# Kernel optimization log

Hardware: AMD Instinct MI355X
Metric: run time of the kernel (lower is better)

## Reference

```python
import jax, jax.numpy as jnp
import numpy as np

EPS = 1e-5
DIM = 1024
HEADS = 8
DIM_HEAD = 64
INNER = HEADS * DIM_HEAD  # 512


def layernorm(x, g, b):
    mu = jnp.mean(x, axis=-1, keepdims=True)
    var = jnp.var(x, axis=-1, keepdims=True)
    return (x - mu) * jax.lax.rsqrt(var + EPS) * g + b


def setup_inputs() -> dict:
    key = jax.random.key(0)
    ks = jax.random.split(key, 5)
    b, t, n, m = 4, 4, 2048, 64
    x = jax.random.normal(ks[0], (b, t, n, DIM), dtype=jnp.float32)
    latents = jax.random.normal(ks[1], (b, t, m, DIM), dtype=jnp.float32)
    Wq = jax.random.normal(ks[2], (DIM, INNER), dtype=jnp.float32) * (DIM ** -0.5)
    Wkv = jax.random.normal(ks[3], (DIM, 2 * INNER), dtype=jnp.float32) * (DIM ** -0.5)
    Wo = jax.random.normal(ks[4], (INNER, DIM), dtype=jnp.float32) * (INNER ** -0.5)
    return {
        "x": x, "latents": latents,
        "g_x": jnp.ones((DIM,), jnp.float32), "b_x": jnp.zeros((DIM,), jnp.float32),
        "g_l": jnp.ones((DIM,), jnp.float32), "b_l": jnp.zeros((DIM,), jnp.float32),
        "Wq": Wq, "Wkv": Wkv, "Wo": Wo,
    }


def reference(x, latents, g_x, b_x, g_l, b_l, Wq, Wkv, Wo):
    b, t, n, d = x.shape
    m = latents.shape[2]
    h, dh = HEADS, DIM_HEAD
    scale = dh ** -0.5

    xn = layernorm(x, g_x, b_x)              # (b,t,n,d)
    ln = layernorm(latents, g_l, b_l)        # (b,t,m,d)

    q = jnp.einsum('btmd,de->btme', ln, Wq)  # (b,t,m,inner)
    kv_in = jnp.concatenate([xn, ln], axis=-2)           # (b,t,n+m,d)
    kv = jnp.einsum('btjd,de->btje', kv_in, Wkv)         # (b,t,n+m,2*inner)
    k, v = jnp.split(kv, 2, axis=-1)

    q = q.reshape(b, t, m, h, dh) * scale
    k = k.reshape(b, t, n + m, h, dh)
    v = v.reshape(b, t, n + m, h, dh)

    sim = jnp.einsum('btihd,btjhd->bhtij', q, k)         # (b,h,t,m,n+m)
    sim = sim - jax.lax.stop_gradient(jnp.max(sim, axis=-1, keepdims=True))
    attn = jax.nn.softmax(sim, axis=-1)
    out = jnp.einsum('bhtij,btjhd->btihd', attn, v)      # (b,t,m,h,dh)
    out = out.reshape(b, t, m, h * dh)
    return jnp.einsum('btme,ed->btmd', out, Wo)          # (b,t,m,d)
```

## Files before the change

kernel.cpp:

```cpp
#include <hip/hip_runtime.h>
#include <cstdint>
#include <cstddef>

typedef __attribute__((ext_vector_type(8))) short short8;
typedef __attribute__((ext_vector_type(4))) short short4v;
typedef __attribute__((ext_vector_type(4))) float f32x4;

__device__ __forceinline__ short f2bf(float f) {
    union { float f; unsigned u; } c; c.f = f;
    unsigned r = c.u + 0x7fffu + ((c.u >> 16) & 1u);
    return (short)(r >> 16);
}

__device__ __forceinline__ void gl2lds16(const void* g, void* l) {
    __builtin_amdgcn_global_load_lds(
        (const __attribute__((address_space(1))) void*)g,
        (__attribute__((address_space(3))) void*)l, 16, 0, 0);
}

__global__ __launch_bounds__(256) void wconv(
    const float* __restrict__ S, short* __restrict__ D, int K, int N, float scale)
{
    __shared__ float t[32][33];
    const int kt = blockIdx.x * 32, nt = blockIdx.y * 32;
    const int x = threadIdx.x & 31, y4 = (threadIdx.x >> 5) * 4;
    for (int i = 0; i < 4; i++)
        t[y4 + i][x] = S[(size_t)(kt + y4 + i) * N + nt + x];
    __syncthreads();
    for (int i = 0; i < 4; i++)
        D[(size_t)(nt + y4 + i) * K + kt + x] = f2bf(t[x][y4 + i] * scale);
}

__global__ __launch_bounds__(256) void ln_kernel(
    const float* __restrict__ x, const float* __restrict__ lat,
    const float* __restrict__ gx, const float* __restrict__ bx,
    const float* __restrict__ gl, const float* __restrict__ bl,
    short* __restrict__ Aout, short* __restrict__ Lq)
{
    const int wave = threadIdx.x >> 6, lane = threadIdx.x & 63;
    const int r = blockIdx.x * 4 + wave;
    const float *src, *g, *b; size_t drow; short* dst2 = nullptr;
    if (r < 32768) {
        int bt = r >> 11, i = r & 2047;
        src = x + (size_t)r * 1024; g = gx; b = bx;
        drow = (size_t)bt * 2112 + i;
    } else {
        int idx = r - 32768;
        int bt = idx >> 6, i = idx & 63;
        src = lat + (size_t)idx * 1024; g = gl; b = bl;
        drow = (size_t)bt * 2112 + 2048 + i;
        dst2 = Lq + (size_t)idx * 1024;
    }
    float4 v[4];
    for (int j = 0; j < 4; j++) v[j] = ((const float4*)src)[lane + 64 * j];
    float s = 0.f, s2 = 0.f;
    for (int j = 0; j < 4; j++) {
        s  += v[j].x + v[j].y + v[j].z + v[j].w;
        s2 += v[j].x * v[j].x + v[j].y * v[j].y + v[j].z * v[j].z + v[j].w * v[j].w;
    }
    for (int off = 32; off >= 1; off >>= 1) { s += __shfl_xor(s, off); s2 += __shfl_xor(s2, off); }
    const float mu   = s * (1.f / 1024.f);
    const float rstd = rsqrtf(s2 * (1.f / 1024.f) - mu * mu + 1e-5f);
    for (int j = 0; j < 4; j++) {
        float4 gv = ((const float4*)g)[lane + 64 * j];
        float4 bv = ((const float4*)b)[lane + 64 * j];
        short4v o;
        o[0] = f2bf((v[j].x - mu) * rstd * gv.x + bv.x);
        o[1] = f2bf((v[j].y - mu) * rstd * gv.y + bv.y);
        o[2] = f2bf((v[j].z - mu) * rstd * gv.z + bv.z);
        o[3] = f2bf((v[j].w - mu) * rstd * gv.w + bv.w);
        *(short4v*)(Aout + drow * 1024 + (size_t)(lane + 64 * j) * 4) = o;
        if (dst2) *(short4v*)(dst2 + (size_t)(lane + 64 * j) * 4) = o;
    }
}

template <typename OutT>
__global__ __launch_bounds__(256) void gemm_bt(
    const short* __restrict__ A, const short* __restrict__ Bt,
    OutT* __restrict__ C, int N, int K)
{
    __shared__ short As[128 * 32];
    __shared__ short Bs[128 * 32];
    const int tid  = threadIdx.x;
    const int wave = tid >> 6, lane = tid & 63;
    const int col  = lane & 15, quad = lane >> 4;
    const int n0 = blockIdx.x * 128, m0 = blockIdx.y * 128;
    const int wm = (wave >> 1) * 64, wn = (wave & 1) * 64;
    const int sr = tid >> 2;
    const int sk = (tid & 3) * 8;

    f32x4 acc[4][4];
    for (int i = 0; i < 4; i++) for (int j = 0; j < 4; j++) acc[i][j] = f32x4{0.f, 0.f, 0.f, 0.f};

    const short* Ar0 = A  + (size_t)(m0 + sr)      * K + sk;
    const short* Ar1 = A  + (size_t)(m0 + sr + 64) * K + sk;
    const short* Br0 = Bt + (size_t)(n0 + sr)      * K + sk;
    const short* Br1 = Bt + (size_t)(n0 + sr + 64) * K + sk;
    short* lA0 = &As[sr * 32 + sk];
    short* lA1 = &As[(sr + 64) * 32 + sk];
    short* lB0 = &Bs[sr * 32 + sk];
    short* lB1 = &Bs[(sr + 64) * 32 + sk];

    for (int k0 = 0; k0 < K; k0 += 32) {
        __syncthreads();
        gl2lds16(Ar0 + k0, lA0);
        gl2lds16(Ar1 + k0, lA1);
        gl2lds16(Br0 + k0, lB0);
        gl2lds16(Br1 + k0, lB1);
        __syncthreads();
        short8 af[4], bf[4];
        for (int mt = 0; mt < 4; mt++) af[mt] = *(const short8*)&As[(wm + mt * 16 + col) * 32 + quad * 8];
        for (int nt = 0; nt < 4; nt++) bf[nt] = *(const short8*)&Bs[(wn + nt * 16 + col) * 32 + quad * 8];
        for (int mt = 0; mt < 4; mt++)
            for (int nt = 0; nt < 4; nt++)
                acc[mt][nt] = __builtin_amdgcn_mfma_f32_16x16x32_bf16(af[mt], bf[nt], acc[mt][nt], 0, 0, 0);
    }
    for (int mt = 0; mt < 4; mt++)
        for (int nt = 0; nt < 4; nt++)
            for (int r = 0; r < 4; r++) {
                int row = m0 + wm + mt * 16 + quad * 4 + r;
                int cc  = n0 + wn + nt * 16 + col;
                float v = acc[mt][nt][r];
                if constexpr (sizeof(OutT) == 2) C[(size_t)row * N + cc] = (OutT)f2bf(v);
                else                             C[(size_t)row * N + cc] = v;
            }
}

__global__ __launch_bounds__(256) void transpose_v(const short* __restrict__ KV, short* __restrict__ Vt)
{
    __shared__ short tile[64 * 68];
    const int bth = blockIdx.y, bt = bth >> 3, h = bth & 7;
    const int jt = blockIdx.x * 64;
    const int tid = threadIdx.x;
    for (int it = 0; it < 2; ++it) {
        int s = tid + it * 256;
        int j = s >> 3, dv = (s & 7) * 8;
        short8 v = *(const short8*)(KV + (size_t)(bt * 2112 + jt + j) * 1024 + 512 + h * 64 + dv);
        short4v lo = {v[0], v[1], v[2], v[3]}, hi = {v[4], v[5], v[6], v[7]};
        *(short4v*)&tile[j * 68 + dv]     = lo;
        *(short4v*)&tile[j * 68 + dv + 4] = hi;
    }
    __syncthreads();
    for (int it = 0; it < 2; ++it) {
        int s = tid + it * 256;
        int d = s >> 3, jv = (s & 7) * 8;
        short8 o;
        for (int jj = 0; jj < 8; jj++) o[jj] = tile[(jv + jj) * 68 + d];
        *(short8*)(Vt + (size_t)(bth * 64 + d) * 2112 + jt + jv) = o;
    }
}

__global__ __launch_bounds__(256) void attn_kernel(
    const short* __restrict__ Q,
    const short* __restrict__ KV,
    const short* __restrict__ Vt,
    float* __restrict__ Opart,
    float* __restrict__ Mp,
    float* __restrict__ Lp)
{
    __shared__ __align__(16) short p_lds[4][64 * 72];
    __shared__ float sm[4][64];
    __shared__ float sl[4][64];
    float* oacc = (float*)&p_lds[0][0];

    const int wg = blockIdx.x;
    const int ck = blockIdx.y;
    const int wgc = wg * 8 + ck;
    const int bt = wg >> 3, h = wg & 7;
    const int tid = threadIdx.x;
    const int wave = tid >> 6, lane = tid & 63;
    const int col = lane & 15, quad = lane >> 4;

    short8 qf[4][2];
    for (int mt = 0; mt < 4; mt++)
        for (int ks = 0; ks < 2; ks++)
            qf[mt][ks] = *(const short8*)(Q + (size_t)(bt * 64 + mt * 16 + col) * 512
                                            + h * 64 + ks * 32 + quad * 8);

    float m_run[4][4], l_run[4][4];
    f32x4 o_acc[4][4];
    for (int mt = 0; mt < 4; mt++)
        for (int r = 0; r < 4; r++) { m_run[mt][r] = -__builtin_inff(); l_run[mt][r] = 0.f; }
    for (int mt = 0; mt < 4; mt++)
        for (int dt = 0; dt < 4; dt++) o_acc[mt][dt] = f32x4{0.f, 0.f, 0.f, 0.f};

    short* pl = p_lds[wave];

    for (int jb = ck * 4 + wave; jb < 33; jb += 32) {
        f32x4 s[4][4];
        for (int mt = 0; mt < 4; mt++) for (int nt = 0; nt < 4; nt++) s[mt][nt] = f32x4{0.f, 0.f, 0.f, 0.f};
        for (int nt = 0; nt < 4; nt++) {
            const int j = jb * 64 + nt * 16 + col;
            const short* kp = KV + (size_t)(bt * 2112 + j) * 1024 + h * 64 + quad * 8;
            short8 k0 = *(const short8*)kp;
            short8 k1 = *(const short8*)(kp + 32);
            for (int mt = 0; mt < 4; mt++) {
                s[mt][nt] = __builtin_amdgcn_mfma_f32_16x16x32_bf16(qf[mt][0], k0, s[mt][nt], 0, 0, 0);
                s[mt][nt] = __builtin_amdgcn_mfma_f32_16x16x32_bf16(qf[mt][1], k1, s[mt][nt], 0, 0, 0);
            }
        }
        for (int mt = 0; mt < 4; mt++)
            for (int r = 0; r < 4; r++) {
                float mx = fmaxf(fmaxf(s[mt][0][r], s[mt][1][r]), fmaxf(s[mt][2][r], s[mt][3][r]));
                for (int off = 8; off >= 1; off >>= 1) mx = fmaxf(mx, __shfl_xor(mx, off));
                float mnew = fmaxf(m_run[mt][r], mx);
                float alpha = __expf(m_run[mt][r] - mnew);
                float rs = 0.f;
                for (int nt = 0; nt < 4; nt++) {
                    float p = __expf(s[mt][nt][r] - mnew);
                    s[mt][nt][r] = p;
                    rs += p;
                }
                for (int off = 8; off >= 1; off >>= 1) rs += __shfl_xor(rs, off);
                m_run[mt][r] = mnew;
                l_run[mt][r] = l_run[mt][r] * alpha + rs;
                for (int dt = 0; dt < 4; dt++) o_acc[mt][dt][r] *= alpha;
            }
        for (int mt = 0; mt < 4; mt++)
            for (int nt = 0; nt < 4; nt++)
                for (int r = 0; r < 4; r++)
                    pl[(mt * 16 + quad * 4 + r) * 72 + nt * 16 + col] = f2bf(s[mt][nt][r]);
        for (int ks = 0; ks < 2; ks++) {
            short8 vf[4];
            for (int dt = 0; dt < 4; dt++)
                vf[dt] = *(const short8*)(Vt + (size_t)(wg * 64 + dt * 16 + col) * 2112
                                             + jb * 64 + ks * 32 + quad * 8);
            for (int mt = 0; mt < 4; mt++) {
                short8 pf = *(const short8*)(pl + (mt * 16 + col) * 72 + ks * 32 + quad * 8);
                for (int dt = 0; dt < 4; dt++)
                    o_acc[mt][dt] = __builtin_amdgcn_mfma_f32_16x16x32_bf16(pf, vf[dt], o_acc[mt][dt], 0, 0, 0);
            }
        }
    }

    if (col == 0)
        for (int mt = 0; mt < 4; mt++)
            for (int r = 0; r < 4; r++) {
                int row = mt * 16 + quad * 4 + r;
                sm[wave][row] = m_run[mt][r];
                sl[wave][row] = l_run[mt][r];
            }
    __syncthreads();
    for (int mt = 0; mt < 4; mt++)
        for (int r = 0; r < 4; r++) {
            int row = mt * 16 + quad * 4 + r;
            float M = fmaxf(fmaxf(sm[0][row], sm[1][row]), fmaxf(sm[2][row], sm[3][row]));
            float L = sl[0][row] * __expf(sm[0][row] - M) + sl[1][row] * __expf(sm[1][row] - M)
                    + sl[2][row] * __expf(sm[2][row] - M) + sl[3][row] * __expf(sm[3][row] - M);
            if (wave == 0 && col == 0) { Mp[wgc * 64 + row] = M; Lp[wgc * 64 + row] = L; }
            float sc = __expf(m_run[mt][r] - M);
            for (int dt = 0; dt < 4; dt++) o_acc[mt][dt][r] *= sc;
        }
    for (int i = tid; i < 64 * 64; i += 256) oacc[i] = 0.f;
    __syncthreads();
    for (int w = 0; w < 4; w++) {
        if (wave == w)
            for (int mt = 0; mt < 4; mt++)
                for (int dt = 0; dt < 4; dt++)
                    for (int r = 0; r < 4; r++)
                        oacc[(mt * 16 + quad * 4 + r) * 64 + dt * 16 + col] += o_acc[mt][dt][r];
        __syncthreads();
    }
    for (int i = tid; i < 64 * 64; i += 256)
        Opart[(size_t)wgc * 4096 + i] = oacc[i];
}

__global__ __launch_bounds__(256) void attn_merge(
    const float* __restrict__ Opart, const float* __restrict__ Mp,
    const float* __restrict__ Lp, short* __restrict__ AttO)
{
    int idx = blockIdx.x * 256 + threadIdx.x;
    int wg = idx >> 12, rd = idx & 4095, row = rd >> 6, d = rd & 63;
    float M = -__builtin_inff();
    for (int c = 0; c < 8; c++) M = fmaxf(M, Mp[(wg * 8 + c) * 64 + row]);
    float L = 0.f, O = 0.f;
    for (int c = 0; c < 8; c++) {
        float e = __expf(Mp[(wg * 8 + c) * 64 + row] - M);
        L += e * Lp[(wg * 8 + c) * 64 + row];
        O += e * Opart[(size_t)(wg * 8 + c) * 4096 + rd];
    }
    int bt = wg >> 3, h = wg & 7;
    AttO[(size_t)(bt * 64 + row) * 512 + h * 64 + d] = f2bf(O / L);
}

extern "C" void kernel_launch(void* const* d_in, const int* in_sizes, int n_in,
                              void* d_out, int out_size, void* d_ws, size_t ws_size,
                              hipStream_t stream)
{
    const float* x   = (const float*)d_in[0];
    const float* lat = (const float*)d_in[1];
    const float* g_x = (const float*)d_in[2];
    const float* b_x = (const float*)d_in[3];
    const float* g_l = (const float*)d_in[4];
    const float* b_l = (const float*)d_in[5];
    const float* Wq  = (const float*)d_in[6];
    const float* Wkv = (const float*)d_in[7];
    const float* Wo  = (const float*)d_in[8];
    float* out = (float*)d_out;

    char* ws = (char*)d_ws;
    size_t off = 0;
    auto alloc = [&](size_t bytes) { char* p = ws + off; off += (bytes + 255) & ~(size_t)255; return p; };
    short* A_kvin = (short*)alloc(33792ull * 1024 * 2);
    short* Lq     = (short*)alloc(1024ull * 1024 * 2);
    short* WkvT   = (short*)alloc(1024ull * 1024 * 2);
    short* WqT    = (short*)alloc(512ull * 1024 * 2);
    short* WoT    = (short*)alloc(1024ull * 512 * 2);
    short* KVb    = (short*)alloc(33792ull * 1024 * 2);
    short* Qb     = (short*)alloc(1024ull * 512 * 2);
    short* AttO   = (short*)alloc(1024ull * 512 * 2);
    short* Vt    = A_kvin;
    char*  sc2   = (char*)A_kvin + 36ull * 1024 * 1024;
    float* Opart = (float*)sc2;
    float* Mp    = (float*)(sc2 + 16777216);
    float* Lp    = (float*)(sc2 + 16777216 + 262144);

    wconv<<<dim3(32, 32), 256, 0, stream>>>(Wkv, WkvT, 1024, 1024, 1.0f);
    wconv<<<dim3(32, 16), 256, 0, stream>>>(Wq,  WqT,  1024, 512,  0.125f);
    wconv<<<dim3(16, 32), 256, 0, stream>>>(Wo,  WoT,  512,  1024, 1.0f);
    ln_kernel<<<8448, 256, 0, stream>>>(x, lat, g_x, b_x, g_l, b_l, A_kvin, Lq);
    gemm_bt<short><<<dim3(8, 132), 256, 0, stream>>>(A_kvin, WkvT, KVb, 1024, 1024);
    gemm_bt<short><<<dim3(8, 132), 256, 0, stream>>>(A_kvin + 16896ull * 1024, WkvT,
                                                     KVb + 16896ull * 1024, 1024, 1024);
    gemm_bt<short><<<dim3(4, 8), 256, 0, stream>>>(Lq, WqT, Qb, 512, 1024);
    transpose_v<<<dim3(33, 128), 256, 0, stream>>>(KVb, Vt);
    attn_kernel<<<dim3(128, 8), 256, 0, stream>>>(Qb, KVb, Vt, Opart, Mp, Lp);
    attn_merge<<<2048, 256, 0, stream>>>(Opart, Mp, Lp, AttO);
    gemm_bt<float><<<dim3(8, 8), 256, 0, stream>>>(AttO, WoT, out, 1024, 512);
}
```

Measured before the change: 456.9 us.

## Merge weight-conversion and KV/Q GEMM launches, halve attention key-split count

The three weight transpose/convert launches are folded into one kernel that picks its matrix from the block index. The KV and Q projection GEMMs become one launch, with the Q tiles as extra blocks, and the KV tile order is swapped so blockIdx.x walks rows. Attention now splits keys into 4 chunks instead of 8, which halves the partial outputs and merge work but leaves fewer blocks to fill the GPU. The aim is less launch overhead and less partial-result traffic.

```diff
diff --git a/kernel.cpp b/kernel.cpp
--- a/kernel.cpp
+++ b/kernel.cpp
@@ -18,11 +18,16 @@
         (__attribute__((address_space(3))) void*)l, 16, 0, 0);
 }
 
-__global__ __launch_bounds__(256) void wconv(
-    const float* __restrict__ S, short* __restrict__ D, int K, int N, float scale)
+__global__ __launch_bounds__(256) void wconv_all(
+    const float* __restrict__ Wq, const float* __restrict__ Wkv, const float* __restrict__ Wo,
+    short* __restrict__ WqT, short* __restrict__ WkvT, short* __restrict__ WoT)
 {
     __shared__ float t[32][33];
-    const int kt = blockIdx.x * 32, nt = blockIdx.y * 32;
+    const int id = blockIdx.x;
+    const float* S; short* D; int K, N, kt, nt; float scale = 1.0f;
+    if (id < 1024)      { S = Wkv; D = WkvT; K = 1024; N = 1024; kt = (id >> 5) * 32;          nt = (id & 31) * 32; }
+    else if (id < 1536) { S = Wq;  D = WqT;  K = 1024; N = 512;  kt = ((id - 1024) >> 4) * 32; nt = ((id - 1024) & 15) * 32; scale = 0.125f; }
+    else                { S = Wo;  D = WoT;  K = 512;  N = 1024; kt = ((id - 1536) >> 5) * 32; nt = ((id - 1536) & 31) * 32; }
     const int x = threadIdx.x & 31, y4 = (threadIdx.x >> 5) * 4;
     for (int i = 0; i < 4; i++)
         t[y4 + i][x] = S[(size_t)(kt + y4 + i) * N + nt + x];
@@ -74,17 +79,75 @@
     }
 }
 
-template <typename OutT>
-__global__ __launch_bounds__(256) void gemm_bt(
-    const short* __restrict__ A, const short* __restrict__ Bt,
-    OutT* __restrict__ C, int N, int K)
+__global__ __launch_bounds__(256) void gemm_kvq(
+    const short* __restrict__ A, const short* __restrict__ Bt, short* __restrict__ C,
+    const short* __restrict__ Aq, const short* __restrict__ Btq, short* __restrict__ Cq)
 {
     __shared__ short As[128 * 32];
     __shared__ short Bs[128 * 32];
     const int tid  = threadIdx.x;
     const int wave = tid >> 6, lane = tid & 63;
     const int col  = lane & 15, quad = lane >> 4;
-    const int n0 = blockIdx.x * 128, m0 = blockIdx.y * 128;
+    const short *pA, *pB; short* pC; int m0, n0, N;
+    if (blockIdx.x < 264) {
+        pA = A; pB = Bt; pC = C; N = 1024;
+        m0 = blockIdx.x * 128; n0 = blockIdx.y * 128;
+    } else {
+        int extra = (blockIdx.x - 264) * 8 + blockIdx.y;
+        pA = Aq; pB = Btq; pC = Cq; N = 512;
+        m0 = (extra >> 2) * 128; n0 = (extra & 3) * 128;
+    }
+    const int K = 1024;
+    const int wm = (wave >> 1) * 64, wn = (wave & 1) * 64;
+    const int sr = tid >> 2;
+    const int sk = (tid & 3) * 8;
+
+    f32x4 acc[4][4];
+    for (int i = 0; i < 4; i++) for (int j = 0; j < 4; j++) acc[i][j] = f32x4{0.f, 0.f, 0.f, 0.f};
+
+    const short* Ar0 = pA + (size_t)(m0 + sr)      * K + sk;
+    const short* Ar1 = pA + (size_t)(m0 + sr + 64) * K + sk;
+    const short* Br0 = pB + (size_t)(n0 + sr)      * K + sk;
+    const short* Br1 = pB + (size_t)(n0 + sr + 64) * K + sk;
+    short* lA0 = &As[sr * 32 + sk];
+    short* lA1 = &As[(sr + 64) * 32 + sk];
+    short* lB0 = &Bs[sr * 32 + sk];
+    short* lB1 = &Bs[(sr + 64) * 32 + sk];
+
+    for (int k0 = 0; k0 < K; k0 += 32) {
+        __syncthreads();
+        gl2lds16(Ar0 + k0, lA0);
+        gl2lds16(Ar1 + k0, lA1);
+        gl2lds16(Br0 + k0, lB0);
+        gl2lds16(Br1 + k0, lB1);
+        __syncthreads();
+        short8 af[4], bf[4];
+        for (int mt = 0; mt < 4; mt++) af[mt] = *(const short8*)&As[(wm + mt * 16 + col) * 32 + quad * 8];
+        for (int nt = 0; nt < 4; nt++) bf[nt] = *(const short8*)&Bs[(wn + nt * 16 + col) * 32 + quad * 8];
+        for (int mt = 0; mt < 4; mt++)
+            for (int nt = 0; nt < 4; nt++)
+                acc[mt][nt] = __builtin_amdgcn_mfma_f32_16x16x32_bf16(af[mt], bf[nt], acc[mt][nt], 0, 0, 0);
+    }
+    for (int mt = 0; mt < 4; mt++)
+        for (int nt = 0; nt < 4; nt++)
+            for (int r = 0; r < 4; r++) {
+                int row = m0 + wm + mt * 16 + quad * 4 + r;
+                int cc  = n0 + wn + nt * 16 + col;
+                pC[(size_t)row * N + cc] = f2bf(acc[mt][nt][r]);
+            }
+}
+
+template <typename OutT>
+__global__ __launch_bounds__(256) void gemm_bt(
+    const short* __restrict__ A, const short* __restrict__ Bt,
+    OutT* __restrict__ C, int N, int K)
+{
+    __shared__ short As[128 * 32];
+    __shared__ short Bs[128 * 32];
+    const int tid  = threadIdx.x;
+    const int wave = tid >> 6, lane = tid & 63;
+    const int col  = lane & 15, quad = lane >> 4;
+    const int m0 = blockIdx.x * 128, n0 = blockIdx.y * 128;
     const int wm = (wave >> 1) * 64, wn = (wave & 1) * 64;
     const int sr = tid >> 2;
     const int sk = (tid & 3) * 8;
@@ -165,7 +228,7 @@
 
     const int wg = blockIdx.x;
     const int ck = blockIdx.y;
-    const int wgc = wg * 8 + ck;
+    const int wgc = wg * 4 + ck;
     const int bt = wg >> 3, h = wg & 7;
     const int tid = threadIdx.x;
     const int wave = tid >> 6, lane = tid & 63;
@@ -186,7 +249,7 @@
 
     short* pl = p_lds[wave];
 
-    for (int jb = ck * 4 + wave; jb < 33; jb += 32) {
+    for (int jb = ck * 4 + wave; jb < 33; jb += 16) {
         f32x4 s[4][4];
         for (int mt = 0; mt < 4; mt++) for (int nt = 0; nt < 4; nt++) s[mt][nt] = f32x4{0.f, 0.f, 0.f, 0.f};
         for (int nt = 0; nt < 4; nt++) {
@@ -272,12 +335,12 @@
     int idx = blockIdx.x * 256 + threadIdx.x;
     int wg = idx >> 12, rd = idx & 4095, row = rd >> 6, d = rd & 63;
     float M = -__builtin_inff();
-    for (int c = 0; c < 8; c++) M = fmaxf(M, Mp[(wg * 8 + c) * 64 + row]);
+    for (int c = 0; c < 4; c++) M = fmaxf(M, Mp[(wg * 4 + c) * 64 + row]);
     float L = 0.f, O = 0.f;
-    for (int c = 0; c < 8; c++) {
-        float e = __expf(Mp[(wg * 8 + c) * 64 + row] - M);
-        L += e * Lp[(wg * 8 + c) * 64 + row];
-        O += e * Opart[(size_t)(wg * 8 + c) * 4096 + rd];
+    for (int c = 0; c < 4; c++) {
+        float e = __expf(Mp[(wg * 4 + c) * 64 + row] - M);
+        L += e * Lp[(wg * 4 + c) * 64 + row];
+        O += e * Opart[(size_t)(wg * 4 + c) * 4096 + rd];
     }
     int bt = wg >> 3, h = wg & 7;
     AttO[(size_t)(bt * 64 + row) * 512 + h * 64 + d] = f2bf(O / L);
@@ -312,19 +375,14 @@
     short* Vt    = A_kvin;
     char*  sc2   = (char*)A_kvin + 36ull * 1024 * 1024;
     float* Opart = (float*)sc2;
-    float* Mp    = (float*)(sc2 + 16777216);
-    float* Lp    = (float*)(sc2 + 16777216 + 262144);
-
-    wconv<<<dim3(32, 32), 256, 0, stream>>>(Wkv, WkvT, 1024, 1024, 1.0f);
-    wconv<<<dim3(32, 16), 256, 0, stream>>>(Wq,  WqT,  1024, 512,  0.125f);
-    wconv<<<dim3(16, 32), 256, 0, stream>>>(Wo,  WoT,  512,  1024, 1.0f);
+    float* Mp    = (float*)(sc2 + 8388608);
+    float* Lp    = (float*)(sc2 + 8388608 + 131072);
+
+    wconv_all<<<2048, 256, 0, stream>>>(Wq, Wkv, Wo, WqT, WkvT, WoT);
     ln_kernel<<<8448, 256, 0, stream>>>(x, lat, g_x, b_x, g_l, b_l, A_kvin, Lq);
-    gemm_bt<short><<<dim3(8, 132), 256, 0, stream>>>(A_kvin, WkvT, KVb, 1024, 1024);
-    gemm_bt<short><<<dim3(8, 132), 256, 0, stream>>>(A_kvin + 16896ull * 1024, WkvT,
-                                                     KVb + 16896ull * 1024, 1024, 1024);
-    gemm_bt<short><<<dim3(4, 8), 256, 0, stream>>>(Lq, WqT, Qb, 512, 1024);
+    gemm_kvq<<<dim3(268, 8), 256, 0, stream>>>(A_kvin, WkvT, KVb, Lq, WqT, Qb);
     transpose_v<<<dim3(33, 128), 256, 0, stream>>>(KVb, Vt);
-    attn_kernel<<<dim3(128, 8), 256, 0, stream>>>(Qb, KVb, Vt, Opart, Mp, Lp);
+    attn_kernel<<<dim3(128, 4), 256, 0, stream>>>(Qb, KVb, Vt, Opart, Mp, Lp);
     attn_merge<<<2048, 256, 0, stream>>>(Opart, Mp, Lp, AttO);
     gemm_bt<float><<<dim3(8, 8), 256, 0, stream>>>(AttO, WoT, out, 1024, 512);
 }
```

New measurement: 388.3 us. 1.18x faster.
